# Kernel optimization log

Hardware: AMD Instinct MI355X
Metric: run time of the kernel (lower is better)

Reference implementation:

```python
import jax, jax.numpy as jnp
import numpy as np

B, S, D = 2, 2048, 2048
H, G, HD = 32, 8, 64  # heads, kv groups, head_dim; group_size = H // G = 4
EPS = 1e-6


def setup_inputs() -> dict:
    key = jax.random.key(0)
    ks = jax.random.split(key, 6)
    x = jax.random.normal(ks[0], (B, S, D), dtype=jnp.float32)
    # causal mask: True = masked out
    mask = jnp.triu(jnp.ones((S, S), dtype=bool), k=1)
    # RoPE tables
    inv_freq = 1.0 / (10000.0 ** (jnp.arange(0, HD, 2, dtype=jnp.float32) / HD))
    ang = jnp.arange(S, dtype=jnp.float32)[:, None] * inv_freq[None, :]  # [S, HD/2]
    cos = jnp.concatenate([jnp.cos(ang), jnp.cos(ang)], axis=-1)  # [S, HD]
    sin = jnp.concatenate([jnp.sin(ang), jnp.sin(ang)], axis=-1)
    Wq = 0.02 * jax.random.normal(ks[1], (H * HD, D), dtype=jnp.float32)
    Wk = 0.02 * jax.random.normal(ks[2], (G * HD, D), dtype=jnp.float32)
    Wv = 0.02 * jax.random.normal(ks[3], (G * HD, D), dtype=jnp.float32)
    Wo = 0.02 * jax.random.normal(ks[4], (D, H * HD), dtype=jnp.float32)
    q_scale = jnp.zeros((HD,), dtype=jnp.float32)  # RMSNorm scale init to zeros
    k_scale = jnp.zeros((HD,), dtype=jnp.float32)
    return {"x": x, "mask": mask, "cos": cos, "sin": sin, "Wq": Wq, "Wk": Wk,
            "Wv": Wv, "Wo": Wo, "q_scale": q_scale, "k_scale": k_scale}


def _rmsnorm(t, scale):
    tf = t.astype(jnp.float32)
    var = jnp.mean(tf * tf, axis=-1, keepdims=True)
    return (tf * jax.lax.rsqrt(var + EPS) * (1.0 + scale)).astype(t.dtype)


def _rope(t, cos, sin):
    # t: [b, h, s, hd]
    s_len, hd = t.shape[2], t.shape[3]
    c = cos[:s_len][None, None]
    s = sin[:s_len][None, None]
    t1, t2 = t[..., : hd // 2], t[..., hd // 2:]
    rotated = jnp.concatenate([-t2, t1], axis=-1)
    return (t * c + rotated * s).astype(t.dtype)


def reference(x, mask, cos, sin, Wq, Wk, Wv, Wo, q_scale, k_scale):
    b, n, _ = x.shape
    gs = H // G  # group size
    q = (x @ Wq.T).reshape(b, n, H, HD).transpose(0, 2, 1, 3)   # [b,H,S,hd]
    k = (x @ Wk.T).reshape(b, n, G, HD).transpose(0, 2, 1, 3)   # [b,G,S,hd]
    v = (x @ Wv.T).reshape(b, n, G, HD).transpose(0, 2, 1, 3)   # [b,G,S,hd]
    q = _rmsnorm(q, q_scale)
    k = _rmsnorm(k, k_scale)
    q = _rope(q, cos, sin)
    k = _rope(k, cos, sin)
    q = q * (HD ** -0.5)
    # GQA broadcast: head h uses kv group h // gs (matches repeat_interleave ordering)
    q5 = q.reshape(b, G, gs, n, HD)
    scores = jnp.einsum('bgmqd,bgkd->bgmqk', q5, k)  # [b,G,gs,S,S]
    scores = jnp.where(mask[None, None, None], -jnp.inf, scores)
    attn = jax.nn.softmax(scores, axis=-1)
    ctx = jnp.einsum('bgmqk,bgkd->bgmqd', attn, v)   # [b,G,gs,S,hd]
    ctx = ctx.reshape(b, H, n, HD).transpose(0, 2, 1, 3).reshape(b, n, H * HD)
    return ctx @ Wo.T
```

## Files before the change

### kernel.cpp

```cpp
#include <hip/hip_runtime.h>
#include <hip/hip_bf16.h>
#include <stdint.h>

constexpr int B  = 2;
constexpr int S  = 2048;
constexpr int D  = 2048;
constexpr int H  = 32;
constexpr int G  = 8;
constexpr int HD = 64;
constexpr float EPS = 1e-6f;

constexpr float LOG2E  = 1.44269504088896341f;
constexpr float C8     = 8.0f * LOG2E;

typedef __attribute__((address_space(1))) const uint32_t  gas_u32;
typedef __attribute__((address_space(3))) uint32_t        las_u32;
typedef __attribute__((ext_vector_type(8))) short  bf16x8;
typedef __attribute__((ext_vector_type(4))) float  f32x4;

static __device__ __forceinline__ unsigned short f2b(float f) {
    __hip_bfloat16 h = __float2bfloat16(f);
    return *reinterpret_cast<unsigned short*>(&h);
}

__global__ __launch_bounds__(256) void conv_f2b(const float* __restrict__ in,
                                                unsigned short* __restrict__ out,
                                                int n4)
{
    int i = blockIdx.x * blockDim.x + threadIdx.x;
    const int stride = gridDim.x * blockDim.x;
    for (; i < n4; i += stride) {
        float4 v = ((const float4*)in)[i];
        ushort4 o;
        o.x = f2b(v.x); o.y = f2b(v.y); o.z = f2b(v.z); o.w = f2b(v.w);
        ((ushort4*)out)[i] = o;
    }
}

__global__ __launch_bounds__(256) void gemm_bf16(const unsigned short* __restrict__ A,
                                                 const unsigned short* __restrict__ Bm,
                                                 float* __restrict__ C,
                                                 int M, int N, int K)
{
    constexpr int BM = 128, BN = 128, BK = 64;
    __shared__ unsigned short As[BM * BK];
    __shared__ unsigned short Bs[BN * BK];

    const int tid  = threadIdx.x;
    const int w    = tid >> 6;
    const int lane = tid & 63;
    const int wr   = w >> 1, wc = w & 1;
    const int bm   = blockIdx.y * BM;
    const int bn   = blockIdx.x * BN;

    f32x4 acc[4][4];
    #pragma unroll
    for (int mi = 0; mi < 4; ++mi)
        #pragma unroll
        for (int ni = 0; ni < 4; ++ni)
            acc[mi][ni] = (f32x4){0.f, 0.f, 0.f, 0.f};

    for (int k0 = 0; k0 < K; k0 += BK) {
        #pragma unroll
        for (int i = 0; i < 4; ++i) {
            const int n  = i * 256 + tid;
            const int r  = n >> 3, cs = n & 7;
            const int cg = cs ^ (r & 7);
            const unsigned short* ga = A + (size_t)(bm + r) * K + k0 + cg * 8;
            __builtin_amdgcn_global_load_lds((gas_u32*)ga,
                (las_u32*)(As + (i * 256 + w * 64) * 8), 16, 0, 0);
        }
        #pragma unroll
        for (int i = 0; i < 4; ++i) {
            const int n  = i * 256 + tid;
            const int r  = n >> 3, cs = n & 7;
            const int cg = cs ^ (r & 7);
            const unsigned short* gb = Bm + (size_t)(bn + r) * K + k0 + cg * 8;
            __builtin_amdgcn_global_load_lds((gas_u32*)gb,
                (las_u32*)(Bs + (i * 256 + w * 64) * 8), 16, 0, 0);
        }
        asm volatile("s_waitcnt vmcnt(0)" ::: "memory");
        __syncthreads();

        #pragma unroll
        for (int ks = 0; ks < 2; ++ks) {
            bf16x8 af[4], bfr[4];
            #pragma unroll
            for (int mi = 0; mi < 4; ++mi) {
                const int r    = wr * 64 + mi * 16 + (lane & 15);
                const int c    = ks * 4 + (lane >> 4);
                const int slot = c ^ (r & 7);
                af[mi] = *(const bf16x8*)(As + r * 64 + slot * 8);
            }
            #pragma unroll
            for (int ni = 0; ni < 4; ++ni) {
                const int r    = wc * 64 + ni * 16 + (lane & 15);
                const int c    = ks * 4 + (lane >> 4);
                const int slot = c ^ (r & 7);
                bfr[ni] = *(const bf16x8*)(Bs + r * 64 + slot * 8);
            }
            #pragma unroll
            for (int mi = 0; mi < 4; ++mi)
                #pragma unroll
                for (int ni = 0; ni < 4; ++ni)
                    acc[mi][ni] = __builtin_amdgcn_mfma_f32_16x16x32_bf16(
                        af[mi], bfr[ni], acc[mi][ni], 0, 0, 0);
        }
        __syncthreads();
    }

    const int col0 = bn + wc * 64 + (lane & 15);
    const int row0 = bm + wr * 64 + (lane >> 4) * 4;
    #pragma unroll
    for (int mi = 0; mi < 4; ++mi)
        #pragma unroll
        for (int ni = 0; ni < 4; ++ni)
            #pragma unroll
            for (int rg = 0; rg < 4; ++rg)
                C[(size_t)(row0 + mi * 16 + rg) * N + (col0 + ni * 16)] =
                    acc[mi][ni][rg];
}

__global__ __launch_bounds__(64) void norm_rope_bf(const float* __restrict__ t,
                                                   unsigned short* __restrict__ o,
                                                   const float* __restrict__ cosb,
                                                   const float* __restrict__ sinb,
                                                   const float* __restrict__ scale,
                                                   int heads, float mulscale)
{
    const int lane = threadIdx.x;
    const int idx  = blockIdx.x;
    const int h    = idx % heads;
    const int m    = idx / heads;
    const int s    = m % S;

    const float* row = t + ((size_t)m * heads + h) * HD;
    float v = row[lane];

    float sq = v * v;
    #pragma unroll
    for (int off = 32; off; off >>= 1) sq += __shfl_xor(sq, off, 64);
    float inv = rsqrtf(sq * (1.0f / HD) + EPS);
    float n = v * inv * (1.0f + scale[lane]);

    float other = __shfl_xor(n, 32, 64);
    float rot   = (lane < 32) ? -other : other;
    float c  = cosb[(size_t)s * HD + lane];
    float sn = sinb[(size_t)s * HD + lane];
    o[((size_t)m * heads + h) * HD + lane] = f2b((n * c + rot * sn) * mulscale);
}

__global__ __launch_bounds__(256) void vtrans(const float* __restrict__ v,
                                              unsigned short* __restrict__ vtb)
{
    __shared__ float tile[64][65];
    const int tid = threadIdx.x;
    const int blk = blockIdx.x;
    const int st  = blk & 31;
    const int g   = (blk >> 5) & 7;
    const int b   = blk >> 8;
    const int s0  = st * 64;

    {
        const int si = tid >> 2;
        const int fc = (tid & 3) * 16;
        const float* src = v + ((size_t)(b * S + s0 + si) * G + g) * HD + fc;
        #pragma unroll
        for (int u = 0; u < 4; ++u) {
            float4 a = ((const float4*)src)[u];
            tile[si][fc + u * 4 + 0] = a.x;
            tile[si][fc + u * 4 + 1] = a.y;
            tile[si][fc + u * 4 + 2] = a.z;
            tile[si][fc + u * 4 + 3] = a.w;
        }
    }
    __syncthreads();
    {
        const int d  = tid >> 2;
        const int sc = (tid & 3) * 16;
        ushort4 o[4];
        #pragma unroll
        for (int u = 0; u < 4; ++u) {
            o[u].x = f2b(tile[sc + u * 4 + 0][d]);
            o[u].y = f2b(tile[sc + u * 4 + 1][d]);
            o[u].z = f2b(tile[sc + u * 4 + 2][d]);
            o[u].w = f2b(tile[sc + u * 4 + 3][d]);
        }
        unsigned short* dst = vtb + ((size_t)(b * G + g) * HD + d) * S + s0 + sc;
        #pragma unroll
        for (int u = 0; u < 4; ++u)
            ((ushort4*)dst)[u] = o[u];
    }
}

__global__ __launch_bounds__(64, 2) void attn_mfma(
    const unsigned short* __restrict__ qb,
    const unsigned short* __restrict__ kb,
    const unsigned short* __restrict__ vtb,
    unsigned short* __restrict__ ctx)
{
    __shared__ unsigned short Kl[2][2048];
    __shared__ unsigned short Vl[2][2048];

    const int lane = threadIdx.x;
    const int g4   = lane >> 4;
    const int l15  = lane & 15;

    const int blk = blockIdx.x;
    const int pr  = blk & 31;
    const int bh  = blk >> 5;
    const int h   = bh & 31;
    const int b   = bh >> 5;
    const int gg  = h >> 2;

    const unsigned short* kbase = kb  + ((size_t)b * S * G + gg) * HD;
    const unsigned short* vbase = vtb + (size_t)(b * G + gg) * HD * S;

    auto stageK = [&](int t, int buf) {
        #pragma unroll
        for (int ii = 0; ii < 4; ++ii) {
            const int n  = ii * 64 + lane;
            const int s  = n >> 3, c = n & 7;
            const int cp = c ^ (s & 7);
            const int key = ((s >> 2) & 3) * 8 + (s & 3) + ((s >> 4) << 2);
            const unsigned short* src = kbase + (size_t)(t * 32 + key) * (G * HD) + cp * 8;
            __builtin_amdgcn_global_load_lds((gas_u32*)src,
                (las_u32*)&Kl[buf][ii * 512], 16, 0, 0);
        }
    };
    auto stageV = [&](int t, int buf) {
        #pragma unroll
        for (int ii = 0; ii < 4; ++ii) {
            const int n  = ii * 64 + lane;
            const int d2 = n >> 3, c = n & 7;
            const int cp = c ^ (d2 & 7);
            const int d  = 2 * d2 + (cp >> 2);
            const unsigned short* src = vbase + (size_t)d * S + t * 32 + (cp & 3) * 8;
            __builtin_amdgcn_global_load_lds((gas_u32*)src,
                (las_u32*)&Vl[buf][ii * 512], 16, 0, 0);
        }
    };

    for (int pass = 0; pass < 2; ++pass) {
        const int qblk = pass ? (63 - pr) : pr;
        const int qb0  = qblk * 32;
        const int nt   = qblk + 1;

        bf16x8 qf[2][2];
        #pragma unroll
        for (int qg = 0; qg < 2; ++qg)
            #pragma unroll
            for (int dc = 0; dc < 2; ++dc)
                qf[qg][dc] = *(const bf16x8*)(qb +
                    ((size_t)(b * S + qb0 + qg * 16 + l15) * H + h) * HD + dc * 32 + g4 * 8);

        f32x4 accO[2][4];
        #pragma unroll
        for (int qg = 0; qg < 2; ++qg)
            #pragma unroll
            for (int dg = 0; dg < 4; ++dg)
                accO[qg][dg] = (f32x4){0.f, 0.f, 0.f, 0.f};
        float lsum[2] = {0.f, 0.f};

        stageK(0, 0); stageV(0, 0);

        for (int t = 0; t < nt; ++t) {
            const int cur = t & 1;
            if (t + 1 < nt) {
                stageK(t + 1, cur ^ 1); stageV(t + 1, cur ^ 1);
                asm volatile("s_waitcnt vmcnt(8)" ::: "memory");
            } else {
                asm volatile("s_waitcnt vmcnt(0)" ::: "memory");
            }

            f32x4 sc[2][2];
            #pragma unroll
            for (int kg = 0; kg < 2; ++kg)
                #pragma unroll
                for (int qg = 0; qg < 2; ++qg)
                    sc[kg][qg] = (f32x4){0.f, 0.f, 0.f, 0.f};
            #pragma unroll
            for (int kg = 0; kg < 2; ++kg) {
                const int srow = l15 + 16 * kg;
                #pragma unroll
                for (int dc = 0; dc < 2; ++dc) {
                    const int ch = (dc * 4 + g4) ^ (srow & 7);
                    bf16x8 kf = *(const bf16x8*)&Kl[cur][srow * 64 + ch * 8];
                    #pragma unroll
                    for (int qg = 0; qg < 2; ++qg)
                        sc[kg][qg] = __builtin_amdgcn_mfma_f32_16x16x32_bf16(
                            kf, qf[qg][dc], sc[kg][qg], 0, 0, 0);
                }
            }

            bf16x8 pf[2];
            #pragma unroll
            for (int qg = 0; qg < 2; ++qg) {
                const int qglob = qb0 + qg * 16 + l15;
                #pragma unroll
                for (int kg = 0; kg < 2; ++kg)
                    #pragma unroll
                    for (int r = 0; r < 4; ++r) {
                        const int kglob = t * 32 + g4 * 8 + kg * 4 + r;
                        float e = exp2f(sc[kg][qg][r] - C8);
                        e = (kglob <= qglob) ? e : 0.f;
                        lsum[qg] += e;
                        pf[qg][kg * 4 + r] = (short)f2b(e);
                    }
            }

            #pragma unroll
            for (int dg = 0; dg < 4; ++dg) {
                const int d2r = (l15 >> 1) + 8 * dg;
                const int ch  = (4 * (l15 & 1) + g4) ^ (d2r & 7);
                bf16x8 vf = *(const bf16x8*)&Vl[cur][d2r * 64 + ch * 8];
                #pragma unroll
                for (int qg = 0; qg < 2; ++qg)
                    accO[qg][dg] = __builtin_amdgcn_mfma_f32_16x16x32_bf16(
                        pf[qg], vf, accO[qg][dg], 0, 0, 0);
            }
        }

        #pragma unroll
        for (int qg = 0; qg < 2; ++qg) {
            lsum[qg] += __shfl_xor(lsum[qg], 16, 64);
            lsum[qg] += __shfl_xor(lsum[qg], 32, 64);
        }
        #pragma unroll
        for (int qg = 0; qg < 2; ++qg)
            #pragma unroll
            for (int r = 0; r < 4; ++r) {
                const float linv = 1.f / __shfl(lsum[qg], g4 * 4 + r, 64);
                const int qrow = qb0 + qg * 16 + g4 * 4 + r;
                unsigned short* crow = ctx + ((size_t)(b * S + qrow) * H + h) * HD + l15;
                #pragma unroll
                for (int dg = 0; dg < 4; ++dg)
                    crow[dg * 16] = f2b(accO[qg][dg][r] * linv);
            }
    }
}

extern "C" void kernel_launch(void* const* d_in, const int* in_sizes, int n_in,
                              void* d_out, int out_size, void* d_ws, size_t ws_size,
                              hipStream_t stream)
{
    const float* x       = (const float*)d_in[0];
    const float* cosb    = (const float*)d_in[2];
    const float* sinb    = (const float*)d_in[3];
    const float* Wq      = (const float*)d_in[4];
    const float* Wk      = (const float*)d_in[5];
    const float* Wv      = (const float*)d_in[6];
    const float* Wo      = (const float*)d_in[7];
    const float* q_scale = (const float*)d_in[8];
    const float* k_scale = (const float*)d_in[9];
    float* out = (float*)d_out;

    unsigned short* wsu = (unsigned short*)d_ws;
    size_t off = 0;
    unsigned short* x_bf   = wsu + off; off += (size_t)B * S * D;
    unsigned short* Wq_bf  = wsu + off; off += (size_t)H * HD * D;
    unsigned short* Wk_bf  = wsu + off; off += (size_t)G * HD * D;
    unsigned short* Wv_bf  = wsu + off; off += (size_t)G * HD * D;
    unsigned short* Wo_bf  = wsu + off; off += (size_t)D * H * HD;
    unsigned short* ctx_bf = wsu + off; off += (size_t)B * S * H * HD;
    float* kbuf = (float*)(wsu + off);
    float* vbuf = kbuf + (size_t)B * S * G * HD;
    float* qbuf = out;
    unsigned short* q_bf = x_bf;
    unsigned short* k_bf = Wq_bf;
    unsigned short* Vt   = Wk_bf;

    const int M = B * S;

    conv_f2b<<<512, 256, 0, stream>>>(x,  x_bf,  (B * S * D) / 4);
    conv_f2b<<<256, 256, 0, stream>>>(Wq, Wq_bf, (H * HD * D) / 4);
    conv_f2b<<<128, 256, 0, stream>>>(Wk, Wk_bf, (G * HD * D) / 4);
    conv_f2b<<<128, 256, 0, stream>>>(Wv, Wv_bf, (G * HD * D) / 4);
    conv_f2b<<<256, 256, 0, stream>>>(Wo, Wo_bf, (D * H * HD) / 4);

    gemm_bf16<<<dim3((H * HD) / 128, M / 128), 256, 0, stream>>>(x_bf, Wq_bf, qbuf, M, H * HD, D);
    gemm_bf16<<<dim3((G * HD) / 128, M / 128), 256, 0, stream>>>(x_bf, Wk_bf, kbuf, M, G * HD, D);
    gemm_bf16<<<dim3((G * HD) / 128, M / 128), 256, 0, stream>>>(x_bf, Wv_bf, vbuf, M, G * HD, D);

    norm_rope_bf<<<M * H, 64, 0, stream>>>(qbuf, q_bf, cosb, sinb, q_scale, H, 0.125f * LOG2E);
    norm_rope_bf<<<M * G, 64, 0, stream>>>(kbuf, k_bf, cosb, sinb, k_scale, G, 1.0f);

    vtrans<<<B * G * 32, 256, 0, stream>>>(vbuf, Vt);

    attn_mfma<<<32 * B * H, 64, 0, stream>>>(q_bf, k_bf, Vt, ctx_bf);

    gemm_bf16<<<dim3(D / 128, M / 128), 256, 0, stream>>>(ctx_bf, Wo_bf, out, M, D, D);
}
```

Before: 459.4 us.

## Fuse weight conversions, K/V GEMMs, norm-rope launches; restructure attention to 4-wave blocks

Merges the four weight conversions into one kernel, computes K and V with a single GEMM into an interleaved buffer, and fuses the Q and K norm/RoPE into one launch of 4 units per block. The attention kernel changes from single-wave blocks that each process two query blocks to 256-thread blocks whose four waves take four adjacent query blocks and share cooperatively staged K/V tiles. It also specialises the diagonal tile so the causal mask only runs there, and adds MFMA priority hints. This cuts launch count and redundant K/V loads, but adds per-tile block barriers, and waves in the same block finish at different tiles, leaving some idle.

```diff
diff --git a/kernel.cpp b/kernel.cpp
--- a/kernel.cpp
+++ b/kernel.cpp
@@ -1,6 +1,7 @@
 #include <hip/hip_runtime.h>
 #include <hip/hip_bf16.h>
 #include <stdint.h>
+#include <type_traits>
 
 constexpr int B  = 2;
 constexpr int S  = 2048;
@@ -37,6 +38,31 @@
     }
 }
 
+__global__ __launch_bounds__(256) void conv_weights(const float* __restrict__ Wq,
+                                                    const float* __restrict__ Wk,
+                                                    const float* __restrict__ Wv,
+                                                    const float* __restrict__ Wo,
+                                                    unsigned short* __restrict__ out)
+{
+    constexpr int c1 = (H * HD * D) / 4;
+    constexpr int c2 = c1 + (G * HD * D) / 4;
+    constexpr int c3 = c2 + (G * HD * D) / 4;
+    constexpr int c4 = c3 + (D * H * HD) / 4;
+
+    int i = blockIdx.x * blockDim.x + threadIdx.x;
+    const int stride = gridDim.x * blockDim.x;
+    for (; i < c4; i += stride) {
+        float4 v;
+        if      (i < c1) v = ((const float4*)Wq)[i];
+        else if (i < c2) v = ((const float4*)Wk)[i - c1];
+        else if (i < c3) v = ((const float4*)Wv)[i - c2];
+        else             v = ((const float4*)Wo)[i - c3];
+        ushort4 o;
+        o.x = f2b(v.x); o.y = f2b(v.y); o.z = f2b(v.z); o.w = f2b(v.w);
+        ((ushort4*)out)[i] = o;
+    }
+}
+
 __global__ __launch_bounds__(256) void gemm_bf16(const unsigned short* __restrict__ A,
                                                  const unsigned short* __restrict__ Bm,
                                                  float* __restrict__ C,
@@ -121,22 +147,42 @@
                     acc[mi][ni][rg];
 }
 
-__global__ __launch_bounds__(64) void norm_rope_bf(const float* __restrict__ t,
-                                                   unsigned short* __restrict__ o,
-                                                   const float* __restrict__ cosb,
-                                                   const float* __restrict__ sinb,
-                                                   const float* __restrict__ scale,
-                                                   int heads, float mulscale)
-{
-    const int lane = threadIdx.x;
-    const int idx  = blockIdx.x;
-    const int h    = idx % heads;
-    const int m    = idx / heads;
-    const int s    = m % S;
-
-    const float* row = t + ((size_t)m * heads + h) * HD;
-    float v = row[lane];
-
+__global__ __launch_bounds__(256) void norm_rope_fused(
+    const float* __restrict__ qsrc,
+    const float* __restrict__ kvsrc,
+    unsigned short* __restrict__ q_bf,
+    unsigned short* __restrict__ k_bf,
+    const float* __restrict__ cosb,
+    const float* __restrict__ sinb,
+    const float* __restrict__ q_scale,
+    const float* __restrict__ k_scale)
+{
+    constexpr int NQ = B * S * H;
+    const int lane = threadIdx.x & 63;
+    const int unit = blockIdx.x * 4 + (threadIdx.x >> 6);
+
+    const float* src;
+    unsigned short* dst;
+    const float* scale;
+    float mulscale;
+    int m;
+    if (unit < NQ) {
+        m = unit >> 5;
+        const int h = unit & 31;
+        src = qsrc + (size_t)m * 2048 + h * 64;
+        dst = q_bf + (size_t)m * 2048 + h * 64;
+        scale = q_scale; mulscale = 0.125f * LOG2E;
+    } else {
+        const int u2 = unit - NQ;
+        m = u2 >> 3;
+        const int g = u2 & 7;
+        src = kvsrc + (size_t)m * 1024 + g * 64;
+        dst = k_bf + (size_t)m * 512 + g * 64;
+        scale = k_scale; mulscale = 1.0f;
+    }
+    const int s = m & (S - 1);
+
+    float v = src[lane];
     float sq = v * v;
     #pragma unroll
     for (int off = 32; off; off >>= 1) sq += __shfl_xor(sq, off, 64);
@@ -147,10 +193,10 @@
     float rot   = (lane < 32) ? -other : other;
     float c  = cosb[(size_t)s * HD + lane];
     float sn = sinb[(size_t)s * HD + lane];
-    o[((size_t)m * heads + h) * HD + lane] = f2b((n * c + rot * sn) * mulscale);
-}
-
-__global__ __launch_bounds__(256) void vtrans(const float* __restrict__ v,
+    dst[lane] = f2b((n * c + rot * sn) * mulscale);
+}
+
+__global__ __launch_bounds__(256) void vtrans(const float* __restrict__ kv,
                                               unsigned short* __restrict__ vtb)
 {
     __shared__ float tile[64][65];
@@ -164,7 +210,7 @@
     {
         const int si = tid >> 2;
         const int fc = (tid & 3) * 16;
-        const float* src = v + ((size_t)(b * S + s0 + si) * G + g) * HD + fc;
+        const float* src = kv + (size_t)(b * S + s0 + si) * 1024 + 512 + g * 64 + fc;
         #pragma unroll
         for (int u = 0; u < 4; ++u) {
             float4 a = ((const float4*)src)[u];
@@ -193,7 +239,7 @@
     }
 }
 
-__global__ __launch_bounds__(64, 2) void attn_mfma(
+__global__ __launch_bounds__(256, 4) void attn_mfma(
     const unsigned short* __restrict__ qb,
     const unsigned short* __restrict__ kb,
     const unsigned short* __restrict__ vtb,
@@ -202,142 +248,144 @@
     __shared__ unsigned short Kl[2][2048];
     __shared__ unsigned short Vl[2][2048];
 
-    const int lane = threadIdx.x;
+    const int tid  = threadIdx.x;
+    const int w    = tid >> 6;
+    const int lane = tid & 63;
     const int g4   = lane >> 4;
     const int l15  = lane & 15;
 
-    const int blk = blockIdx.x;
-    const int pr  = blk & 31;
-    const int bh  = blk >> 5;
-    const int h   = bh & 31;
-    const int b   = bh >> 5;
-    const int gg  = h >> 2;
+    const int blk  = blockIdx.x;
+    const int bh   = blk & 63;
+    const int j    = 15 - (blk >> 6);
+    const int h    = bh & 31;
+    const int b    = bh >> 5;
+    const int gg   = h >> 2;
+
+    const int qblk  = 4 * j + w;
+    const int qb0   = qblk * 32;
+    const int ntmax = 4 * j + 4;
 
     const unsigned short* kbase = kb  + ((size_t)b * S * G + gg) * HD;
     const unsigned short* vbase = vtb + (size_t)(b * G + gg) * HD * S;
 
     auto stageK = [&](int t, int buf) {
-        #pragma unroll
-        for (int ii = 0; ii < 4; ++ii) {
-            const int n  = ii * 64 + lane;
-            const int s  = n >> 3, c = n & 7;
-            const int cp = c ^ (s & 7);
-            const int key = ((s >> 2) & 3) * 8 + (s & 3) + ((s >> 4) << 2);
-            const unsigned short* src = kbase + (size_t)(t * 32 + key) * (G * HD) + cp * 8;
-            __builtin_amdgcn_global_load_lds((gas_u32*)src,
-                (las_u32*)&Kl[buf][ii * 512], 16, 0, 0);
-        }
+        const int n  = w * 64 + lane;
+        const int s  = n >> 3, c = n & 7;
+        const int cp = c ^ (s & 7);
+        const int key = ((s >> 2) & 3) * 8 + (s & 3) + ((s >> 4) << 2);
+        const unsigned short* src = kbase + (size_t)(t * 32 + key) * (G * HD) + cp * 8;
+        __builtin_amdgcn_global_load_lds((gas_u32*)src,
+            (las_u32*)&Kl[buf][w * 512], 16, 0, 0);
     };
     auto stageV = [&](int t, int buf) {
-        #pragma unroll
-        for (int ii = 0; ii < 4; ++ii) {
-            const int n  = ii * 64 + lane;
-            const int d2 = n >> 3, c = n & 7;
-            const int cp = c ^ (d2 & 7);
-            const int d  = 2 * d2 + (cp >> 2);
-            const unsigned short* src = vbase + (size_t)d * S + t * 32 + (cp & 3) * 8;
-            __builtin_amdgcn_global_load_lds((gas_u32*)src,
-                (las_u32*)&Vl[buf][ii * 512], 16, 0, 0);
-        }
+        const int n  = w * 64 + lane;
+        const int d2 = n >> 3, c = n & 7;
+        const int cp = c ^ (d2 & 7);
+        const int d  = 2 * d2 + (cp >> 2);
+        const unsigned short* src = vbase + (size_t)d * S + t * 32 + (cp & 3) * 8;
+        __builtin_amdgcn_global_load_lds((gas_u32*)src,
+            (las_u32*)&Vl[buf][w * 512], 16, 0, 0);
     };
 
-    for (int pass = 0; pass < 2; ++pass) {
-        const int qblk = pass ? (63 - pr) : pr;
-        const int qb0  = qblk * 32;
-        const int nt   = qblk + 1;
-
-        bf16x8 qf[2][2];
-        #pragma unroll
-        for (int qg = 0; qg < 2; ++qg)
-            #pragma unroll
-            for (int dc = 0; dc < 2; ++dc)
-                qf[qg][dc] = *(const bf16x8*)(qb +
-                    ((size_t)(b * S + qb0 + qg * 16 + l15) * H + h) * HD + dc * 32 + g4 * 8);
-
-        f32x4 accO[2][4];
-        #pragma unroll
-        for (int qg = 0; qg < 2; ++qg)
-            #pragma unroll
-            for (int dg = 0; dg < 4; ++dg)
-                accO[qg][dg] = (f32x4){0.f, 0.f, 0.f, 0.f};
-        float lsum[2] = {0.f, 0.f};
-
-        stageK(0, 0); stageV(0, 0);
-
-        for (int t = 0; t < nt; ++t) {
-            const int cur = t & 1;
-            if (t + 1 < nt) {
-                stageK(t + 1, cur ^ 1); stageV(t + 1, cur ^ 1);
-                asm volatile("s_waitcnt vmcnt(8)" ::: "memory");
-            } else {
-                asm volatile("s_waitcnt vmcnt(0)" ::: "memory");
+    bf16x8 qf[2][2];
+    #pragma unroll
+    for (int qg = 0; qg < 2; ++qg)
+        #pragma unroll
+        for (int dc = 0; dc < 2; ++dc)
+            qf[qg][dc] = *(const bf16x8*)(qb +
+                ((size_t)(b * S + qb0 + qg * 16 + l15) * H + h) * HD + dc * 32 + g4 * 8);
+
+    f32x4 accO[2][4];
+    #pragma unroll
+    for (int qg = 0; qg < 2; ++qg)
+        #pragma unroll
+        for (int dg = 0; dg < 4; ++dg)
+            accO[qg][dg] = (f32x4){0.f, 0.f, 0.f, 0.f};
+    float lsum[2] = {0.f, 0.f};
+
+    auto tile_body = [&](int t, int cur, auto DIAG) {
+        constexpr bool diag = decltype(DIAG)::value;
+
+        f32x4 sc[2][2];
+        #pragma unroll
+        for (int kg = 0; kg < 2; ++kg)
+            #pragma unroll
+            for (int qg = 0; qg < 2; ++qg)
+                sc[kg][qg] = (f32x4){0.f, 0.f, 0.f, 0.f};
+        __builtin_amdgcn_s_setprio(1);
+        #pragma unroll
+        for (int kg = 0; kg < 2; ++kg) {
+            const int srow = l15 + 16 * kg;
+            #pragma unroll
+            for (int dc = 0; dc < 2; ++dc) {
+                const int ch = (dc * 4 + g4) ^ (srow & 7);
+                bf16x8 kf = *(const bf16x8*)&Kl[cur][srow * 64 + ch * 8];
+                #pragma unroll
+                for (int qg = 0; qg < 2; ++qg)
+                    sc[kg][qg] = __builtin_amdgcn_mfma_f32_16x16x32_bf16(
+                        kf, qf[qg][dc], sc[kg][qg], 0, 0, 0);
             }
-
-            f32x4 sc[2][2];
+        }
+        __builtin_amdgcn_s_setprio(0);
+
+        bf16x8 pf[2];
+        #pragma unroll
+        for (int qg = 0; qg < 2; ++qg) {
+            const int qglob = qb0 + qg * 16 + l15;
             #pragma unroll
             for (int kg = 0; kg < 2; ++kg)
                 #pragma unroll
-                for (int qg = 0; qg < 2; ++qg)
-                    sc[kg][qg] = (f32x4){0.f, 0.f, 0.f, 0.f};
-            #pragma unroll
-            for (int kg = 0; kg < 2; ++kg) {
-                const int srow = l15 + 16 * kg;
-                #pragma unroll
-                for (int dc = 0; dc < 2; ++dc) {
-                    const int ch = (dc * 4 + g4) ^ (srow & 7);
-                    bf16x8 kf = *(const bf16x8*)&Kl[cur][srow * 64 + ch * 8];
-                    #pragma unroll
-                    for (int qg = 0; qg < 2; ++qg)
-                        sc[kg][qg] = __builtin_amdgcn_mfma_f32_16x16x32_bf16(
-                            kf, qf[qg][dc], sc[kg][qg], 0, 0, 0);
+                for (int r = 0; r < 4; ++r) {
+                    float e = exp2f(sc[kg][qg][r] - C8);
+                    if constexpr (diag) {
+                        const int kglob = t * 32 + g4 * 8 + kg * 4 + r;
+                        e = (kglob <= qglob) ? e : 0.f;
+                    }
+                    lsum[qg] += e;
+                    pf[qg][kg * 4 + r] = (short)f2b(e);
                 }
-            }
-
-            bf16x8 pf[2];
-            #pragma unroll
-            for (int qg = 0; qg < 2; ++qg) {
-                const int qglob = qb0 + qg * 16 + l15;
-                #pragma unroll
-                for (int kg = 0; kg < 2; ++kg)
-                    #pragma unroll
-                    for (int r = 0; r < 4; ++r) {
-                        const int kglob = t * 32 + g4 * 8 + kg * 4 + r;
-                        float e = exp2f(sc[kg][qg][r] - C8);
-                        e = (kglob <= qglob) ? e : 0.f;
-                        lsum[qg] += e;
-                        pf[qg][kg * 4 + r] = (short)f2b(e);
-                    }
-            }
-
-            #pragma unroll
-            for (int dg = 0; dg < 4; ++dg) {
-                const int d2r = (l15 >> 1) + 8 * dg;
-                const int ch  = (4 * (l15 & 1) + g4) ^ (d2r & 7);
-                bf16x8 vf = *(const bf16x8*)&Vl[cur][d2r * 64 + ch * 8];
-                #pragma unroll
-                for (int qg = 0; qg < 2; ++qg)
-                    accO[qg][dg] = __builtin_amdgcn_mfma_f32_16x16x32_bf16(
-                        pf[qg], vf, accO[qg][dg], 0, 0, 0);
-            }
-        }
-
-        #pragma unroll
-        for (int qg = 0; qg < 2; ++qg) {
-            lsum[qg] += __shfl_xor(lsum[qg], 16, 64);
-            lsum[qg] += __shfl_xor(lsum[qg], 32, 64);
-        }
-        #pragma unroll
-        for (int qg = 0; qg < 2; ++qg)
-            #pragma unroll
-            for (int r = 0; r < 4; ++r) {
-                const float linv = 1.f / __shfl(lsum[qg], g4 * 4 + r, 64);
-                const int qrow = qb0 + qg * 16 + g4 * 4 + r;
-                unsigned short* crow = ctx + ((size_t)(b * S + qrow) * H + h) * HD + l15;
-                #pragma unroll
-                for (int dg = 0; dg < 4; ++dg)
-                    crow[dg * 16] = f2b(accO[qg][dg][r] * linv);
-            }
-    }
+        }
+
+        __builtin_amdgcn_s_setprio(1);
+        #pragma unroll
+        for (int dg = 0; dg < 4; ++dg) {
+            const int d2r = (l15 >> 1) + 8 * dg;
+            const int ch  = (4 * (l15 & 1) + g4) ^ (d2r & 7);
+            bf16x8 vf = *(const bf16x8*)&Vl[cur][d2r * 64 + ch * 8];
+            #pragma unroll
+            for (int qg = 0; qg < 2; ++qg)
+                accO[qg][dg] = __builtin_amdgcn_mfma_f32_16x16x32_bf16(
+                    pf[qg], vf, accO[qg][dg], 0, 0, 0);
+        }
+        __builtin_amdgcn_s_setprio(0);
+    };
+
+    stageK(0, 0); stageV(0, 0);
+
+    for (int t = 0; t < ntmax; ++t) {
+        const int cur = t & 1;
+        __syncthreads();
+        if (t + 1 < ntmax) { stageK(t + 1, cur ^ 1); stageV(t + 1, cur ^ 1); }
+        if (t < qblk)       tile_body(t, cur, std::false_type{});
+        else if (t == qblk) tile_body(t, cur, std::true_type{});
+    }
+
+    #pragma unroll
+    for (int qg = 0; qg < 2; ++qg) {
+        lsum[qg] += __shfl_xor(lsum[qg], 16, 64);
+        lsum[qg] += __shfl_xor(lsum[qg], 32, 64);
+    }
+    #pragma unroll
+    for (int qg = 0; qg < 2; ++qg)
+        #pragma unroll
+        for (int r = 0; r < 4; ++r) {
+            const float linv = 1.f / __shfl(lsum[qg], g4 * 4 + r, 64);
+            const int qrow = qb0 + qg * 16 + g4 * 4 + r;
+            unsigned short* crow = ctx + ((size_t)(b * S + qrow) * H + h) * HD + l15;
+            #pragma unroll
+            for (int dg = 0; dg < 4; ++dg)
+                crow[dg * 16] = f2b(accO[qg][dg][r] * linv);
+        }
 }
 
 extern "C" void kernel_launch(void* const* d_in, const int* in_sizes, int n_in,
@@ -363,8 +411,7 @@
     unsigned short* Wv_bf  = wsu + off; off += (size_t)G * HD * D;
     unsigned short* Wo_bf  = wsu + off; off += (size_t)D * H * HD;
     unsigned short* ctx_bf = wsu + off; off += (size_t)B * S * H * HD;
-    float* kbuf = (float*)(wsu + off);
-    float* vbuf = kbuf + (size_t)B * S * G * HD;
+    float* kvbuf = (float*)(wsu + off);
     float* qbuf = out;
     unsigned short* q_bf = x_bf;
     unsigned short* k_bf = Wq_bf;
@@ -372,22 +419,18 @@
 
     const int M = B * S;
 
-    conv_f2b<<<512, 256, 0, stream>>>(x,  x_bf,  (B * S * D) / 4);
-    conv_f2b<<<256, 256, 0, stream>>>(Wq, Wq_bf, (H * HD * D) / 4);
-    conv_f2b<<<128, 256, 0, stream>>>(Wk, Wk_bf, (G * HD * D) / 4);
-    conv_f2b<<<128, 256, 0, stream>>>(Wv, Wv_bf, (G * HD * D) / 4);
-    conv_f2b<<<256, 256, 0, stream>>>(Wo, Wo_bf, (D * H * HD) / 4);
-
-    gemm_bf16<<<dim3((H * HD) / 128, M / 128), 256, 0, stream>>>(x_bf, Wq_bf, qbuf, M, H * HD, D);
-    gemm_bf16<<<dim3((G * HD) / 128, M / 128), 256, 0, stream>>>(x_bf, Wk_bf, kbuf, M, G * HD, D);
-    gemm_bf16<<<dim3((G * HD) / 128, M / 128), 256, 0, stream>>>(x_bf, Wv_bf, vbuf, M, G * HD, D);
-
-    norm_rope_bf<<<M * H, 64, 0, stream>>>(qbuf, q_bf, cosb, sinb, q_scale, H, 0.125f * LOG2E);
-    norm_rope_bf<<<M * G, 64, 0, stream>>>(kbuf, k_bf, cosb, sinb, k_scale, G, 1.0f);
-
-    vtrans<<<B * G * 32, 256, 0, stream>>>(vbuf, Vt);
-
-    attn_mfma<<<32 * B * H, 64, 0, stream>>>(q_bf, k_bf, Vt, ctx_bf);
+    conv_f2b<<<512, 256, 0, stream>>>(x, x_bf, (B * S * D) / 4);
+    conv_weights<<<512, 256, 0, stream>>>(Wq, Wk, Wv, Wo, Wq_bf);
+
+    gemm_bf16<<<dim3(2048 / 128, M / 128), 256, 0, stream>>>(x_bf, Wq_bf, qbuf, M, 2048, D);
+    gemm_bf16<<<dim3(1024 / 128, M / 128), 256, 0, stream>>>(x_bf, Wk_bf, kvbuf, M, 1024, D);
+
+    norm_rope_fused<<<(M * (H + G)) / 4, 256, 0, stream>>>(
+        qbuf, kvbuf, q_bf, k_bf, cosb, sinb, q_scale, k_scale);
+
+    vtrans<<<B * G * 32, 256, 0, stream>>>(kvbuf, Vt);
+
+    attn_mfma<<<16 * B * H / 4 * 4, 256, 0, stream>>>(q_bf, k_bf, Vt, ctx_bf);
 
     gemm_bf16<<<dim3(D / 128, M / 128), 256, 0, stream>>>(ctx_bf, Wo_bf, out, M, D, D);
 }
```

New measurement: 376.3 us. 18.1% less time.
